# Kernel optimization log

Hardware: AMD Instinct MI355X
Metric: run time of the kernel (lower is better)

The kernel has to match this reference:

```python
import jax, jax.numpy as jnp
import numpy as np

CAPACITY_FACTOR = 1.0

def setup_inputs() -> dict:
    key = jax.random.key(0)
    ks = jax.random.split(key, 5)
    B, S, D, E, F = 2, 2048, 1024, 8, 4096
    x = jax.random.normal(ks[0], (B, S, D), dtype=jnp.float32)
    Ws = jax.random.normal(ks[1], (D, E), dtype=jnp.float32) * (1.0 / np.sqrt(D))
    bs = jnp.zeros((E,), dtype=jnp.float32)
    W1 = jax.random.normal(ks[2], (E, D, F), dtype=jnp.float32) * (1.0 / np.sqrt(D))
    b1 = jnp.zeros((E, F), dtype=jnp.float32)
    W2 = jax.random.normal(ks[3], (E, F, D), dtype=jnp.float32) * (1.0 / np.sqrt(F))
    b2 = jnp.zeros((E, D), dtype=jnp.float32)
    return {"x": x, "Ws": Ws, "bs": bs, "W1": W1, "b1": b1, "W2": W2, "b2": b2}

def reference(x, Ws, bs, W1, b1, W2, b2):
    B, S, D = x.shape
    E = Ws.shape[1]
    N = B * S
    k = int(CAPACITY_FACTOR * N / E)  # expert-choice capacity
    xf = x.reshape(N, D)
    # switch gating: [N, E] -> [E, N]
    route_prob = jax.nn.softmax(xf @ Ws + bs, axis=-1).T
    # expert-choice top-k tokens per expert: values/indices [E, k]
    route_vals, routes = jax.lax.top_k(route_prob, k)
    # dispatch: gather per-expert token blocks [E, k, D]
    xin = xf[routes]
    # per-expert FFN (grouped GEMM): Linear -> GELU -> Linear
    h = jax.nn.gelu(jnp.einsum('ekd,edf->ekf', xin, W1) + b1[:, None, :])
    out = jnp.einsum('ekf,efd->ekd', h, W2) + b2[:, None, :]
    # scale by routing prob (is_scale_prob=True)
    out = out * route_vals[..., None]
    # combine: scatter-add into token buffer (== sum over the E-indexed zero tensor)
    final = jnp.zeros((N, D), dtype=x.dtype).at[routes.reshape(-1)].add(out.reshape(-1, D))
    return final.reshape(B, S, D)
```

## Files before the change

kernel.cpp:

```cpp
#include <hip/hip_runtime.h>
#include <hip/hip_bf16.h>

#define N_TOK 4096
#define DIM   1024
#define NEXP  8
#define FDIM  4096
#define KCAP  512

typedef __attribute__((ext_vector_type(8))) short bf16x8;
typedef __attribute__((ext_vector_type(4))) float floatx4;

__device__ inline unsigned short f2bf(float f) {
  union { float f; unsigned int i; } v; v.f = f;
  unsigned int r = v.i + 0x7fffu + ((v.i >> 16) & 1u);
  return (unsigned short)(r >> 16);
}

__device__ inline void ld2lds16(const void* g, void* l) {
  __builtin_amdgcn_global_load_lds(
      (const __attribute__((address_space(1))) unsigned int*)g,
      (__attribute__((address_space(3))) unsigned int*)l,
      16, 0, 0);
}

__global__ __launch_bounds__(512, 1)
void tbig_kernel(const float* __restrict__ src, unsigned short* __restrict__ dst,
                 int R, int C, int ncb) {
  __shared__ unsigned short tile[65536];
  int t = threadIdx.x;
  int bid = blockIdx.x;
  int e = bid >> 6, rem = bid & 63;
  int rb = rem / ncb, cb = rem - rb * ncb;
  size_t off = (size_t)e * R * C;
  int r0 = rb * 256, c0 = cb * 256;
  const float* S = src + off + (size_t)r0 * C + c0;
  unsigned short* D = dst + off + (size_t)c0 * R + r0;

  int wd = t >> 6;
  int f0 = (t & 63) * 4;
  unsigned int* t32 = (unsigned int*)tile;
#pragma unroll 4
  for (int p = 0; p < 32; p++) {
    int d = p * 8 + wd;
    float4 v = *(const float4*)&S[(size_t)d * C + f0];
    unsigned int s = ((unsigned int)(d >> 3) & 31u) << 1;
    unsigned int lo = (unsigned int)f2bf(v.x) | ((unsigned int)f2bf(v.y) << 16);
    unsigned int hi = (unsigned int)f2bf(v.z) | ((unsigned int)f2bf(v.w) << 16);
    t32[(d * 256 + (f0 ^ s)) >> 1] = lo;
    t32[(d * 256 + ((f0 + 2) ^ s)) >> 1] = hi;
  }
  __syncthreads();
  int d0 = (t & 31) * 8;
  unsigned int s = ((unsigned int)(t & 31)) << 1;
  int fl = t >> 5;
#pragma unroll 4
  for (int j = 0; j < 16; j++) {
    int f = j * 16 + fl;
    int base = d0 * 256 + (f ^ (int)s);
    bf16x8 o;
#pragma unroll
    for (int u = 0; u < 8; u++) o[u] = (short)tile[base + u * 256];
    *(bf16x8*)&D[(size_t)f * R + d0] = o;
  }
}

__global__ __launch_bounds__(256)
void router_kernel(const float* __restrict__ x,
                   const float* __restrict__ Ws,
                   const float* __restrict__ bs,
                   float* __restrict__ probs_t,
                   unsigned short* __restrict__ xb) {
  int t = threadIdx.x;
  int token = blockIdx.x * 4 + (t >> 6);
  int lane  = t & 63;
  const float* xr = x + (size_t)token * DIM;
  unsigned short* xbr = xb + (size_t)token * DIM;
  double acc[NEXP];
#pragma unroll
  for (int e = 0; e < NEXP; e++) acc[e] = 0.0;
#pragma unroll
  for (int c = 0; c < 4; c++) {
    int d0 = (c * 64 + lane) * 4;
    float4 xv = *(const float4*)&xr[d0];
    ushort4 ob;
    ob.x = f2bf(xv.x); ob.y = f2bf(xv.y); ob.z = f2bf(xv.z); ob.w = f2bf(xv.w);
    *(ushort4*)&xbr[d0] = ob;
    float xa[4] = {xv.x, xv.y, xv.z, xv.w};
#pragma unroll
    for (int q = 0; q < 4; q++) {
      const float* wr = &Ws[(size_t)(d0 + q) * NEXP];
      float4 w0 = *(const float4*)&wr[0];
      float4 w1 = *(const float4*)&wr[4];
      double xs = (double)xa[q];
      acc[0] += xs * (double)w0.x; acc[1] += xs * (double)w0.y;
      acc[2] += xs * (double)w0.z; acc[3] += xs * (double)w0.w;
      acc[4] += xs * (double)w1.x; acc[5] += xs * (double)w1.y;
      acc[6] += xs * (double)w1.z; acc[7] += xs * (double)w1.w;
    }
  }
#pragma unroll
  for (int off = 32; off > 0; off >>= 1)
#pragma unroll
    for (int e = 0; e < NEXP; e++) acc[e] += __shfl_down(acc[e], off, 64);
  if (lane == 0) {
    double mx = -1e300;
#pragma unroll
    for (int e = 0; e < NEXP; e++) { acc[e] += (double)bs[e]; if (acc[e] > mx) mx = acc[e]; }
    double s = 0.0, p[NEXP];
#pragma unroll
    for (int e = 0; e < NEXP; e++) { p[e] = exp(acc[e] - mx); s += p[e]; }
#pragma unroll
    for (int e = 0; e < NEXP; e++) probs_t[(size_t)e * N_TOK + token] = (float)(p[e] / s);
  }
}

__global__ __launch_bounds__(1024)
void topk_kernel(const float* __restrict__ probs_t, int* __restrict__ routes,
                 float* __restrict__ vals, int* __restrict__ counts,
                 int* __restrict__ inv) {
  int e = blockIdx.x;
  const float* P = probs_t + (size_t)e * N_TOK;
  __shared__ int hist[4096];
  __shared__ int hist2[4096];
  __shared__ int scan[1024];
  __shared__ int sB, sR, sCnt;
  __shared__ unsigned int sPrefix, sMask;
  int t = threadIdx.x;

  float vv[4];
  unsigned int vb[4];
  float4 v4 = *(const float4*)&P[t * 4];
  vv[0] = v4.x; vv[1] = v4.y; vv[2] = v4.z; vv[3] = v4.w;
#pragma unroll
  for (int q = 0; q < 4; q++) vb[q] = __float_as_uint(vv[q]);

  if (t == 0) { sR = KCAP; sPrefix = 0u; sMask = 0u; sCnt = 0; }
  __syncthreads();

  for (int level = 0; level < 3; level++) {
    int nb    = (level < 2) ? 4096 : 256;
    int shift = (level == 0) ? 20 : (level == 1) ? 8 : 0;
    for (int i = t; i < nb; i += 1024) hist[i] = 0;
    __syncthreads();
    unsigned int msk = sMask, pfx = sPrefix;
#pragma unroll
    for (int q = 0; q < 4; q++)
      if ((vb[q] & msk) == pfx)
        atomicAdd(&hist[(vb[q] >> shift) & (nb - 1)], 1);
    __syncthreads();
    int* src = hist; int* dst = hist2;
    for (int d = 1; d < nb; d <<= 1) {
      for (int i = t; i < nb; i += 1024)
        dst[i] = src[i] + ((i + d < nb) ? src[i + d] : 0);
      int* tmp = src; src = dst; dst = tmp;
      __syncthreads();
    }
    int R = sR;
    for (int i = t; i < nb; i += 1024) {
      int si = src[i];
      int sn = (i + 1 < nb) ? src[i + 1] : 0;
      if (si >= R && sn < R) sB = i;
    }
    __syncthreads();
    if (t == 0) {
      int B = sB;
      int strict = (B + 1 < nb) ? src[B + 1] : 0;
      sR = sR - strict;
      sPrefix |= ((unsigned int)B) << shift;
      sMask   |= ((unsigned int)(nb - 1)) << shift;
    }
    __syncthreads();
  }

  unsigned int T = sPrefix;
  int R = sR;
  int cnt = 0;
#pragma unroll
  for (int q = 0; q < 4; q++) if (vb[q] == T) cnt++;
  scan[t] = cnt;
  __syncthreads();
  for (int d = 1; d < 1024; d <<= 1) {
    int v = (t >= d) ? scan[t - d] : 0;
    __syncthreads();
    scan[t] += v;
    __syncthreads();
  }
  int grank = scan[t] - cnt;
#pragma unroll
  for (int q = 0; q < 4; q++) {
    bool sel = false;
    if (vb[q] > T) sel = true;
    else if (vb[q] == T) { if (grank < R) sel = true; grank++; }
    if (sel) {
      int pos = atomicAdd(&sCnt, 1);
      int slot = e * KCAP + pos;
      int token = t * 4 + q;
      routes[slot] = token;
      vals[slot]   = vv[q];
      int pc = atomicAdd(&counts[token], 1);
      inv[token * NEXP + pc] = slot;
    }
  }
}

__global__ __launch_bounds__(256, 3)
void gemm1_kernel(const unsigned short* __restrict__ xb,
                  const unsigned short* __restrict__ w1t,
                  const float* __restrict__ b1,
                  const int* __restrict__ routes,
                  unsigned short* __restrict__ h) {
  int lb = blockIdx.x;
  int sb = ((lb & 7) << 7) | (lb >> 3);
  int nt = sb & 31, mt = (sb >> 5) & 3, e = sb >> 7;
  __shared__ unsigned short smem[16384];
  unsigned short* As = smem;
  unsigned short* Bs = smem + 8192;
  int t = threadIdx.x, lane = t & 63, wave = t >> 6;
  int wm = (wave >> 1) * 64, wn = (wave & 1) * 64;
  int fr = lane & 15, fq = lane >> 4;
  int lrow = lane >> 3, lchunk = (lane & 7) ^ (lrow & 7);
  int sw = fr & 7;

  const unsigned short* aP[4];
  const unsigned short* bP[4];
#pragma unroll
  for (int q = 0; q < 4; q++) {
    int m = wave * 4 + q;
    int row = m * 8 + lrow;
    int token = routes[e * KCAP + mt * 128 + row];
    aP[q] = xb + (size_t)token * DIM + lchunk * 8;
    bP[q] = w1t + ((size_t)e * FDIM + nt * 128 + row) * DIM + lchunk * 8;
  }

  floatx4 acc[4][4];
#pragma unroll
  for (int i = 0; i < 4; i++)
#pragma unroll
    for (int j = 0; j < 4; j++) acc[i][j] = (floatx4)0.0f;

  for (int k0 = 0; k0 < DIM; k0 += 64) {
    __syncthreads();
#pragma unroll
    for (int q = 0; q < 4; q++) {
      int m = wave * 4 + q;
      ld2lds16(aP[q] + k0, As + m * 512);
      ld2lds16(bP[q] + k0, Bs + m * 512);
    }
    __syncthreads();
#pragma unroll
    for (int ks = 0; ks < 2; ks++) {
      bf16x8 af[4], bf[4];
      int cs = ((ks << 2) | fq) ^ sw;
#pragma unroll
      for (int i = 0; i < 4; i++)
        af[i] = *(const bf16x8*)&As[(wm + i * 16 + fr) * 64 + cs * 8];
#pragma unroll
      for (int j = 0; j < 4; j++)
        bf[j] = *(const bf16x8*)&Bs[(wn + j * 16 + fr) * 64 + cs * 8];
#pragma unroll
      for (int i = 0; i < 4; i++)
#pragma unroll
        for (int j = 0; j < 4; j++)
          acc[i][j] = __builtin_amdgcn_mfma_f32_16x16x32_bf16(af[i], bf[j], acc[i][j], 0, 0, 0);
    }
  }

  float bias[4];
#pragma unroll
  for (int j = 0; j < 4; j++) bias[j] = b1[e * FDIM + nt * 128 + wn + j * 16 + fr];
  float* LC = (float*)smem;
#pragma unroll
  for (int p = 0; p < 2; p++) {
    __syncthreads();
    if ((wn >> 6) == p) {
#pragma unroll
      for (int i = 0; i < 4; i++)
#pragma unroll
        for (int r = 0; r < 4; r++) {
          int lr = wm + i * 16 + fq * 4 + r;
#pragma unroll
          for (int j = 0; j < 4; j++) {
            float v = acc[i][j][r] + bias[j];
            float u = 0.7978845608028654f * (v + 0.044715f * v * v * v);
            LC[lr * 64 + j * 16 + fr] = v * __builtin_amdgcn_rcpf(1.0f + __expf(-2.0f * u));
          }
        }
    }
    __syncthreads();
    int row = t >> 1, ch = (t & 1) * 32;
    size_t hb = (((size_t)e * 64 + nt * 2 + p) * KCAP + mt * 128 + row) * 64 + ch;
    const float* lrow2 = &LC[row * 64 + ch];
#pragma unroll
    for (int qq = 0; qq < 4; qq++) {
      bf16x8 o;
#pragma unroll
      for (int u8 = 0; u8 < 8; u8++) o[u8] = (short)f2bf(lrow2[qq * 8 + u8]);
      *(bf16x8*)&h[hb + qq * 8] = o;
    }
  }
}

__global__ __launch_bounds__(256, 3)
void gemm2_kernel(const unsigned short* __restrict__ h,
                  const unsigned short* __restrict__ w2t,
                  const float* __restrict__ b2,
                  const float* __restrict__ vals,
                  float* __restrict__ partials) {
  int lb = blockIdx.x;
  int sb = ((lb & 7) << 6) | (lb >> 3);
  int nt = sb & 7, mt = (sb >> 3) & 3, z = sb >> 5;
  int e = z >> 1, s = z & 1;
  __shared__ unsigned short smem[16384];
  unsigned short* As = smem;
  unsigned short* Bs = smem + 8192;
  int t = threadIdx.x, lane = t & 63, wave = t >> 6;
  int wm = (wave >> 1) * 64, wn = (wave & 1) * 64;
  int fr = lane & 15, fq = lane >> 4;
  int lrow = lane >> 3, lchunk = (lane & 7) ^ (lrow & 7);
  int sw = fr & 7;

  const unsigned short* aP[4];
  const unsigned short* bP[4];
#pragma unroll
  for (int q = 0; q < 4; q++) {
    int m = wave * 4 + q;
    int row = m * 8 + lrow;
    aP[q] = h + (((size_t)e * 64 + s * 32) * KCAP + mt * 128 + row) * 64 + lchunk * 8;
    bP[q] = w2t + ((size_t)e * DIM + nt * 128 + row) * FDIM + s * 2048 + lchunk * 8;
  }

  floatx4 acc[4][4];
#pragma unroll
  for (int i = 0; i < 4; i++)
#pragma unroll
    for (int j = 0; j < 4; j++) acc[i][j] = (floatx4)0.0f;

  for (int k0 = 0; k0 < 2048; k0 += 64) {
    __syncthreads();
#pragma unroll
    for (int q = 0; q < 4; q++) {
      int m = wave * 4 + q;
      ld2lds16(aP[q] + (size_t)k0 * 512, As + m * 512);
      ld2lds16(bP[q] + k0, Bs + m * 512);
    }
    __syncthreads();
#pragma unroll
    for (int ks = 0; ks < 2; ks++) {
      bf16x8 af[4], bf[4];
      int cs = ((ks << 2) | fq) ^ sw;
#pragma unroll
      for (int i = 0; i < 4; i++)
        af[i] = *(const bf16x8*)&As[(wm + i * 16 + fr) * 64 + cs * 8];
#pragma unroll
      for (int j = 0; j < 4; j++)
        bf[j] = *(const bf16x8*)&Bs[(wn + j * 16 + fr) * 64 + cs * 8];
#pragma unroll
      for (int i = 0; i < 4; i++)
#pragma unroll
        for (int j = 0; j < 4; j++)
          acc[i][j] = __builtin_amdgcn_mfma_f32_16x16x32_bf16(af[i], bf[j], acc[i][j], 0, 0, 0);
    }
  }

  float* LC = (float*)smem;
  float* outp = partials + (size_t)s * N_TOK * DIM;
  int slotbase = e * KCAP + mt * 128;
  float bias[4];
#pragma unroll
  for (int j = 0; j < 4; j++)
    bias[j] = (s == 0) ? b2[e * DIM + nt * 128 + wn + j * 16 + fr] : 0.0f;
#pragma unroll
  for (int p = 0; p < 2; p++) {
    __syncthreads();
    if ((wn >> 6) == p) {
#pragma unroll
      for (int i = 0; i < 4; i++)
#pragma unroll
        for (int r = 0; r < 4; r++) {
          int lr = wm + i * 16 + fq * 4 + r;
          float vs = vals[slotbase + lr];
#pragma unroll
          for (int j = 0; j < 4; j++)
            LC[lr * 64 + j * 16 + fr] = (acc[i][j][r] + bias[j]) * vs;
        }
    }
    __syncthreads();
    int row = t >> 1, ch = (t & 1) * 32;
    float* dst = outp + (size_t)(slotbase + row) * DIM + nt * 128 + p * 64 + ch;
#pragma unroll
    for (int qq = 0; qq < 8; qq++)
      *(float4*)&dst[qq * 4] = *(const float4*)&LC[row * 64 + ch + qq * 4];
  }
}

__global__ __launch_bounds__(256)
void combine_kernel(const float* __restrict__ partials, const int* __restrict__ counts,
                    const int* __restrict__ inv, float* __restrict__ out) {
  int token = blockIdx.x;
  int t = threadIdx.x;
  int c = counts[token];
  float4 acc = {0.f, 0.f, 0.f, 0.f};
  for (int i = 0; i < c; i++) {
    int slot = inv[token * NEXP + i];
    const float* base = partials + (size_t)slot * DIM + t * 4;
#pragma unroll
    for (int s = 0; s < 2; s++) {
      float4 v = *(const float4*)&base[(size_t)s * N_TOK * DIM];
      acc.x += v.x; acc.y += v.y; acc.z += v.z; acc.w += v.w;
    }
  }
  *(float4*)&out[(size_t)token * DIM + t * 4] = acc;
}

extern "C" void kernel_launch(void* const* d_in, const int* in_sizes, int n_in,
                              void* d_out, int out_size, void* d_ws, size_t ws_size,
                              hipStream_t stream) {
  const float* x  = (const float*)d_in[0];
  const float* Ws = (const float*)d_in[1];
  const float* bs = (const float*)d_in[2];
  const float* W1 = (const float*)d_in[3];
  const float* b1 = (const float*)d_in[4];
  const float* W2 = (const float*)d_in[5];
  const float* b2 = (const float*)d_in[6];
  float* out = (float*)d_out;

  char* ws = (char*)d_ws;
  unsigned short* wt = (unsigned short*)ws; ws += (size_t)NEXP * FDIM * DIM * 2;
  unsigned short* h  = (unsigned short*)ws; ws += (size_t)NEXP * KCAP * FDIM * 2;
  char* pshare = ws; ws += (size_t)2 * N_TOK * DIM * 4;
  unsigned short* xb = (unsigned short*)pshare;
  float* partials    = (float*)pshare;
  float* probs  = (float*)ws; ws += (size_t)NEXP * N_TOK * 4;
  int*   routes = (int*)ws;   ws += NEXP * KCAP * 4;
  float* vals   = (float*)ws; ws += NEXP * KCAP * 4;
  int*   counts = (int*)ws;   ws += N_TOK * 4;
  int*   inv    = (int*)ws;   ws += N_TOK * NEXP * 4;

  hipMemsetAsync(counts, 0, N_TOK * sizeof(int), stream);
  tbig_kernel<<<512, 512, 0, stream>>>(W1, wt, DIM, FDIM, 16);
  router_kernel<<<1024, 256, 0, stream>>>(x, Ws, bs, probs, xb);
  topk_kernel<<<NEXP, 1024, 0, stream>>>(probs, routes, vals, counts, inv);
  gemm1_kernel<<<1024, 256, 0, stream>>>(xb, wt, b1, routes, h);
  tbig_kernel<<<512, 512, 0, stream>>>(W2, wt, FDIM, DIM, 4);
  gemm2_kernel<<<512, 256, 0, stream>>>(h, wt, b2, vals, partials);
  combine_kernel<<<N_TOK, 256, 0, stream>>>(partials, counts, inv, out);
}
```

Baseline: 460.5 us.

## Fuse weight transposes with router and top-k kernels to overlap work

```diff
diff --git a/kernel.cpp b/kernel.cpp
--- a/kernel.cpp
+++ b/kernel.cpp
@@ -23,25 +23,25 @@
       16, 0, 0);
 }
 
-__global__ __launch_bounds__(512, 1)
-void tbig_kernel(const float* __restrict__ src, unsigned short* __restrict__ dst,
-                 int R, int C, int ncb) {
-  __shared__ unsigned short tile[65536];
-  int t = threadIdx.x;
-  int bid = blockIdx.x;
-  int e = bid >> 6, rem = bid & 63;
+template<int NT>
+__device__ inline void tbig_body(const float* __restrict__ src,
+                                 unsigned short* __restrict__ dst,
+                                 int R, int C, int ncb, int b, int t,
+                                 unsigned short* tile) {
+  int e = b >> 6, rem = b & 63;
   int rb = rem / ncb, cb = rem - rb * ncb;
   size_t off = (size_t)e * R * C;
   int r0 = rb * 256, c0 = cb * 256;
   const float* S = src + off + (size_t)r0 * C + c0;
   unsigned short* D = dst + off + (size_t)c0 * R + r0;
 
+  constexpr int RP = NT / 64;
   int wd = t >> 6;
   int f0 = (t & 63) * 4;
   unsigned int* t32 = (unsigned int*)tile;
 #pragma unroll 4
-  for (int p = 0; p < 32; p++) {
-    int d = p * 8 + wd;
+  for (int p = 0; p < 256 / RP; p++) {
+    int d = p * RP + wd;
     float4 v = *(const float4*)&S[(size_t)d * C + f0];
     unsigned int s = ((unsigned int)(d >> 3) & 31u) << 1;
     unsigned int lo = (unsigned int)f2bf(v.x) | ((unsigned int)f2bf(v.y) << 16);
@@ -52,10 +52,11 @@
   __syncthreads();
   int d0 = (t & 31) * 8;
   unsigned int s = ((unsigned int)(t & 31)) << 1;
+  constexpr int FL = NT / 32;
   int fl = t >> 5;
 #pragma unroll 4
-  for (int j = 0; j < 16; j++) {
-    int f = j * 16 + fl;
+  for (int j = 0; j < 256 / FL; j++) {
+    int f = j * FL + fl;
     int base = d0 * 256 + (f ^ (int)s);
     bf16x8 o;
 #pragma unroll
@@ -64,14 +65,23 @@
   }
 }
 
-__global__ __launch_bounds__(256)
-void router_kernel(const float* __restrict__ x,
+__global__ __launch_bounds__(512)
+void fused1_kernel(const float* __restrict__ W1, unsigned short* __restrict__ wt,
+                   const float* __restrict__ x,
                    const float* __restrict__ Ws,
                    const float* __restrict__ bs,
                    float* __restrict__ probs_t,
                    unsigned short* __restrict__ xb) {
+  __shared__ unsigned short tile[65536];
+  int bid = blockIdx.x;
   int t = threadIdx.x;
-  int token = blockIdx.x * 4 + (t >> 6);
+
+  if (bid < 512) {
+    tbig_body<512>(W1, wt, DIM, FDIM, 16, bid, t, tile);
+    return;
+  }
+
+  int token = (bid - 512) * 8 + (t >> 6);
   int lane  = t & 63;
   const float* xr = x + (size_t)token * DIM;
   unsigned short* xbr = xb + (size_t)token * DIM;
@@ -115,17 +125,26 @@
 }
 
 __global__ __launch_bounds__(1024)
-void topk_kernel(const float* __restrict__ probs_t, int* __restrict__ routes,
-                 float* __restrict__ vals, int* __restrict__ counts,
-                 int* __restrict__ inv) {
-  int e = blockIdx.x;
-  const float* P = probs_t + (size_t)e * N_TOK;
-  __shared__ int hist[4096];
-  __shared__ int hist2[4096];
-  __shared__ int scan[1024];
+void fused2_kernel(const float* __restrict__ probs_t, int* __restrict__ routes,
+                   float* __restrict__ vals, int* __restrict__ counts,
+                   int* __restrict__ inv,
+                   const float* __restrict__ W2, unsigned short* __restrict__ w2t) {
+  __shared__ int shmem[32768];
   __shared__ int sB, sR, sCnt;
   __shared__ unsigned int sPrefix, sMask;
   int t = threadIdx.x;
+  int bid = blockIdx.x;
+
+  if (bid >= 8) {
+    tbig_body<1024>(W2, w2t, FDIM, DIM, 4, bid - 8, t, (unsigned short*)shmem);
+    return;
+  }
+
+  int e = bid;
+  const float* P = probs_t + (size_t)e * N_TOK;
+  int* hist  = shmem;
+  int* hist2 = shmem + 4096;
+  int* scan  = shmem + 8192;
 
   float vv[4];
   unsigned int vb[4];
@@ -425,8 +444,9 @@
   float* out = (float*)d_out;
 
   char* ws = (char*)d_ws;
-  unsigned short* wt = (unsigned short*)ws; ws += (size_t)NEXP * FDIM * DIM * 2;
-  unsigned short* h  = (unsigned short*)ws; ws += (size_t)NEXP * KCAP * FDIM * 2;
+  unsigned short* wt  = (unsigned short*)ws; ws += (size_t)NEXP * FDIM * DIM * 2;
+  unsigned short* w2t = (unsigned short*)ws; ws += (size_t)NEXP * DIM * FDIM * 2;
+  unsigned short* h   = (unsigned short*)ws; ws += (size_t)NEXP * KCAP * FDIM * 2;
   char* pshare = ws; ws += (size_t)2 * N_TOK * DIM * 4;
   unsigned short* xb = (unsigned short*)pshare;
   float* partials    = (float*)pshare;
@@ -437,11 +457,9 @@
   int*   inv    = (int*)ws;   ws += N_TOK * NEXP * 4;
 
   hipMemsetAsync(counts, 0, N_TOK * sizeof(int), stream);
-  tbig_kernel<<<512, 512, 0, stream>>>(W1, wt, DIM, FDIM, 16);
-  router_kernel<<<1024, 256, 0, stream>>>(x, Ws, bs, probs, xb);
-  topk_kernel<<<NEXP, 1024, 0, stream>>>(probs, routes, vals, counts, inv);
+  fused1_kernel<<<1024, 512, 0, stream>>>(W1, wt, x, Ws, bs, probs, xb);
+  fused2_kernel<<<520, 1024, 0, stream>>>(probs, routes, vals, counts, inv, W2, w2t);
   gemm1_kernel<<<1024, 256, 0, stream>>>(xb, wt, b1, routes, h);
-  tbig_kernel<<<512, 512, 0, stream>>>(W2, wt, FDIM, DIM, 4);
-  gemm2_kernel<<<512, 256, 0, stream>>>(h, wt, b2, vals, partials);
+  gemm2_kernel<<<512, 256, 0, stream>>>(h, w2t, b2, vals, partials);
   combine_kernel<<<N_TOK, 256, 0, stream>>>(partials, counts, inv, out);
 }
```

After: 466.2 us. About the same (+1.2%).
